# Kernel tuning notes

Hardware: AMD Instinct MI355X
Metric: run time of the kernel (lower is better)

The kernel has to match this reference:

```python
import jax, jax.numpy as jnp
import numpy as np

EMBED = 1024
DFF = 4096


def _layernorm(x, g, b, eps=1e-5):
    mu = jnp.mean(x, axis=-1, keepdims=True)
    var = jnp.var(x, axis=-1, keepdims=True)
    return (x - mu) * jax.lax.rsqrt(var + eps) * g + b


def setup_inputs() -> dict:
    key = jax.random.key(0)
    ks = jax.random.split(key, 14)
    s = 1.0 / np.sqrt(EMBED)
    sf = 1.0 / np.sqrt(DFF)
    d = {
        "src": jax.random.normal(ks[0], (4, 2048, EMBED), dtype=jnp.float32),
        "Wq": jax.random.uniform(ks[1], (EMBED, EMBED), jnp.float32, -s, s),
        "bq": jnp.zeros((EMBED,), jnp.float32),
        "Wk": jax.random.uniform(ks[2], (EMBED, EMBED), jnp.float32, -s, s),
        "bk": jnp.zeros((EMBED,), jnp.float32),
        "Wv": jax.random.uniform(ks[3], (EMBED, EMBED), jnp.float32, -s, s),
        "bv": jnp.zeros((EMBED,), jnp.float32),
        "Wo": jax.random.uniform(ks[4], (EMBED, EMBED), jnp.float32, -s, s),
        "bo": jnp.zeros((EMBED,), jnp.float32),
        "W1": jax.random.uniform(ks[5], (EMBED, DFF), jnp.float32, -s, s),
        "b1": jnp.zeros((DFF,), jnp.float32),
        "W2": jax.random.uniform(ks[6], (DFF, EMBED), jnp.float32, -sf, sf),
        "b2": jnp.zeros((EMBED,), jnp.float32),
        "g1": jnp.ones((EMBED,), jnp.float32),
        "be1": jnp.zeros((EMBED,), jnp.float32),
        "g2": jnp.ones((EMBED,), jnp.float32),
        "be2": jnp.zeros((EMBED,), jnp.float32),
    }
    return d


def reference(src, Wq, bq, Wk, bk, Wv, bv, Wo, bo, W1, b1, W2, b2, g1, be1, g2, be2):
    # Q/K/V projections: [b, s, d]
    Q = src @ Wq + bq
    K = src @ Wk + bk
    V = src @ Wv + bv
    # Single-head, UNSCALED attention (faithful to source: no 1/sqrt(d), num_heads unused)
    scores = jnp.einsum("bqd,bkd->bqk", Q, K)  # [b, s, s]
    weights = jax.nn.softmax(scores, axis=-1)
    attn = jnp.einsum("bqk,bkd->bqd", weights, V)
    attn = attn @ Wo + bo
    x = _layernorm(src + attn, g1, be1)
    ff = jax.nn.relu(x @ W1 + b1) @ W2 + b2
    return _layernorm(x + ff, g2, be2)
```

## Files before the change

kernel.cpp:

```cpp
#include <hip/hip_runtime.h>
#include <stdint.h>

typedef unsigned short u16;
typedef _Float16 v8h __attribute__((ext_vector_type(8)));
typedef float v4f __attribute__((ext_vector_type(4)));

static __device__ __forceinline__ float h2f(u16 u) {
    union { u16 s; _Float16 h; } v; v.s = u; return (float)v.h;
}
static __device__ __forceinline__ u16 f2h(float f) {
    union { u16 s; _Float16 h; } v; v.h = (_Float16)f; return v.s;
}

static __device__ __forceinline__ void gload_lds16(const u16* g, const u16* l) {
    __builtin_amdgcn_global_load_lds(
        (const __attribute__((address_space(1))) uint32_t*)(uintptr_t)g,
        (__attribute__((address_space(3))) uint32_t*)(uintptr_t)l,
        16, 0, 0);
}

__global__ __launch_bounds__(256) void cvt_f16(const float* __restrict__ in,
                                               u16* __restrict__ out, int n8) {
    const int i = blockIdx.x * 256 + threadIdx.x;
    if (i >= n8) return;
    const float4 a = ((const float4*)in)[2 * i];
    const float4 b = ((const float4*)in)[2 * i + 1];
    u16 o[8] = {f2h(a.x), f2h(a.y), f2h(a.z), f2h(a.w),
                f2h(b.x), f2h(b.y), f2h(b.z), f2h(b.w)};
    *(uint4*)(out + (size_t)i * 8) = *(const uint4*)o;
}

__global__ __launch_bounds__(256) void transpose_all(
    const float* __restrict__ Wq, const float* __restrict__ Wk,
    const float* __restrict__ Wv, const float* __restrict__ Wo,
    const float* __restrict__ W1, const float* __restrict__ W2,
    u16* __restrict__ WqkvT, u16* __restrict__ WoT,
    u16* __restrict__ W1T, u16* __restrict__ W2T)
{
    int t = blockIdx.x;
    const float* in; u16* out; long ldi, ldo; int xt;
    if (t < 1024)      {            in = Wq; out = WqkvT;               ldi = 1024; ldo = 1024; xt = 32; }
    else if (t < 2048) { t -= 1024; in = Wk; out = WqkvT + 1024*1024;   ldi = 1024; ldo = 1024; xt = 32; }
    else if (t < 3072) { t -= 2048; in = Wv; out = WqkvT + 2*1024*1024; ldi = 1024; ldo = 1024; xt = 32; }
    else if (t < 4096) { t -= 3072; in = Wo; out = WoT;                 ldi = 1024; ldo = 1024; xt = 32; }
    else if (t < 8192) { t -= 4096; in = W1; out = W1T;                 ldi = 4096; ldo = 1024; xt = 128; }
    else               { t -= 8192; in = W2; out = W2T;                 ldi = 1024; ldo = 4096; xt = 32; }
    const int c0 = (t % xt) * 32, r0 = (t / xt) * 32;
    __shared__ float tile[32][33];
    for (int i = threadIdx.y; i < 32; i += 8)
        tile[i][threadIdx.x] = in[(long)(r0 + i) * ldi + c0 + threadIdx.x];
    __syncthreads();
    for (int i = threadIdx.y; i < 32; i += 8)
        out[(long)(c0 + i) * ldo + r0 + threadIdx.x] = f2h(tile[threadIdx.x][i]);
}

template<int OMODE, int BIAS, bool RELU, int NX, int NY, int NZ>
__global__ __launch_bounds__(256, 2) void gemm256n(
    const u16* __restrict__ A, long lda, long Asb,
    const u16* __restrict__ B, long ldb, long Bsb,
    void* __restrict__ Cv, long ldc, long Csb, u16* __restrict__ C1,
    const float* __restrict__ bias, const float* __restrict__ bias2,
    const float* __restrict__ bias3, int K)
{
    constexpr int NWG = NX * NY * NZ;
    static_assert(NWG % 8 == 0, "XCD swizzle needs nwg % 8 == 0");
    alignas(16) __shared__ u16 As[4 * 8192];
    alignas(16) __shared__ u16 Bs[2 * 4096];

    const int tid = threadIdx.x;
    const int lane = tid & 63, wave = tid >> 6;
    const int l16 = lane & 15, quad = lane >> 4;
    const int wm = wave >> 1;
    const int wn = wave & 1;

    const int lin = blockIdx.x;
    const int tl = (lin & 7) * (NWG / 8) + (lin >> 3);
    const int xe = tl % NX;
    const int ye = (tl / NX) % NY;
    const int zb = tl / (NX * NY);
    const long m0 = (long)ye * 256;
    const long n0 = (long)xe * 128;

    const u16* Aop = A + (long)zb * Asb;
    const u16* Bop = B + (long)zb * Bsb;

    const int srow = tid >> 2;
    const int sq = (tid & 3) ^ ((tid >> 3) & 3);
    const long gaofs0 = (m0 + srow) * lda + sq * 8;
    const long gbofs0 = (n0 + srow) * ldb + sq * 8;
    const int wv512n = wave * 512;

    const int swzE = (quad ^ ((l16 >> 1) & 3)) * 8;
    const int aRow = (wm * 128 + l16) * 32 + swzE;
    const int bRow = (wn * 64 + l16) * 32 + swzE;

    v4f acc[8][4];
#pragma unroll
    for (int i = 0; i < 8; ++i)
#pragma unroll
        for (int j = 0; j < 4; ++j)
            acc[i][j] = (v4f){0.f, 0.f, 0.f, 0.f};
    v8h bf[4];

#define STAGE_A(RIDX, KP) do { \
        u16* lb_ = As + (RIDX) * 8192 + wv512n; \
        gload_lds16(Aop + gaofs0 + (KP), lb_); \
        gload_lds16(Aop + gaofs0 + 64 * lda + (KP), lb_ + 2048); \
        gload_lds16(Aop + gaofs0 + 128 * lda + (KP), lb_ + 4096); \
        gload_lds16(Aop + gaofs0 + 192 * lda + (KP), lb_ + 6144); } while (0)
#define STAGE_B(SLOT, KP) do { \
        u16* lb_ = Bs + (SLOT) * 4096 + wv512n; \
        gload_lds16(Bop + gbofs0 + (KP), lb_); \
        gload_lds16(Bop + gbofs0 + 64 * ldb + (KP), lb_ + 2048); } while (0)

#define PHASE(BUF, KH, CH, EVENW, STG) { \
        const u16* Ar_ = As + ((BUF) * 2 + (KH)) * 8192 + aRow + (CH) * 2048; \
        v8h af0 = *(const v8h*)(Ar_); \
        v8h af1 = *(const v8h*)(Ar_ + 512); \
        v8h af2 = *(const v8h*)(Ar_ + 1024); \
        v8h af3 = *(const v8h*)(Ar_ + 1536); \
        if ((CH) == 0) { \
            const u16* Br_ = Bs + (KH) * 4096 + bRow; \
            bf[0] = *(const v8h*)(Br_); \
            bf[1] = *(const v8h*)(Br_ + 512); \
            bf[2] = *(const v8h*)(Br_ + 1024); \
            bf[3] = *(const v8h*)(Br_ + 1536); \
        } \
        STG; \
        __builtin_amdgcn_s_barrier(); \
        asm volatile("s_waitcnt lgkmcnt(0)" ::: "memory"); \
        __builtin_amdgcn_s_setprio(1); \
        acc[(CH)*4+0][0] = __builtin_amdgcn_mfma_f32_16x16x32_f16(af0, bf[0], acc[(CH)*4+0][0], 0, 0, 0); \
        acc[(CH)*4+0][1] = __builtin_amdgcn_mfma_f32_16x16x32_f16(af0, bf[1], acc[(CH)*4+0][1], 0, 0, 0); \
        acc[(CH)*4+0][2] = __builtin_amdgcn_mfma_f32_16x16x32_f16(af0, bf[2], acc[(CH)*4+0][2], 0, 0, 0); \
        acc[(CH)*4+0][3] = __builtin_amdgcn_mfma_f32_16x16x32_f16(af0, bf[3], acc[(CH)*4+0][3], 0, 0, 0); \
        acc[(CH)*4+1][0] = __builtin_amdgcn_mfma_f32_16x16x32_f16(af1, bf[0], acc[(CH)*4+1][0], 0, 0, 0); \
        acc[(CH)*4+1][1] = __builtin_amdgcn_mfma_f32_16x16x32_f16(af1, bf[1], acc[(CH)*4+1][1], 0, 0, 0); \
        acc[(CH)*4+1][2] = __builtin_amdgcn_mfma_f32_16x16x32_f16(af1, bf[2], acc[(CH)*4+1][2], 0, 0, 0); \
        acc[(CH)*4+1][3] = __builtin_amdgcn_mfma_f32_16x16x32_f16(af1, bf[3], acc[(CH)*4+1][3], 0, 0, 0); \
        acc[(CH)*4+2][0] = __builtin_amdgcn_mfma_f32_16x16x32_f16(af2, bf[0], acc[(CH)*4+2][0], 0, 0, 0); \
        acc[(CH)*4+2][1] = __builtin_amdgcn_mfma_f32_16x16x32_f16(af2, bf[1], acc[(CH)*4+2][1], 0, 0, 0); \
        acc[(CH)*4+2][2] = __builtin_amdgcn_mfma_f32_16x16x32_f16(af2, bf[2], acc[(CH)*4+2][2], 0, 0, 0); \
        acc[(CH)*4+2][3] = __builtin_amdgcn_mfma_f32_16x16x32_f16(af2, bf[3], acc[(CH)*4+2][3], 0, 0, 0); \
        acc[(CH)*4+3][0] = __builtin_amdgcn_mfma_f32_16x16x32_f16(af3, bf[0], acc[(CH)*4+3][0], 0, 0, 0); \
        acc[(CH)*4+3][1] = __builtin_amdgcn_mfma_f32_16x16x32_f16(af3, bf[1], acc[(CH)*4+3][1], 0, 0, 0); \
        acc[(CH)*4+3][2] = __builtin_amdgcn_mfma_f32_16x16x32_f16(af3, bf[2], acc[(CH)*4+3][2], 0, 0, 0); \
        acc[(CH)*4+3][3] = __builtin_amdgcn_mfma_f32_16x16x32_f16(af3, bf[3], acc[(CH)*4+3][3], 0, 0, 0); \
        __builtin_amdgcn_s_setprio(0); \
        if (EVENW) asm volatile("s_waitcnt vmcnt(6)" ::: "memory"); \
        __builtin_amdgcn_s_barrier(); \
    }

    STAGE_A(0, 0);  STAGE_B(0, 0);
    STAGE_A(1, 32); STAGE_B(1, 32);
    STAGE_A(2, 64);
    asm volatile("s_waitcnt vmcnt(10)" ::: "memory");
    __builtin_amdgcn_s_barrier();

    const int NT = K >> 7;
#pragma unroll 1
    for (int t = 0; t < NT; ++t) {
        const long kb = (long)t * 128;
        long kp2  = kb + 128; if (kp2  >= K) kp2  = 0;
        long kp2b = kb + 160; if (kp2b >= K) kp2b = 0;
        long kp3  = kb + 192; if (kp3  >= K) kp3  = 0;

        PHASE(0, 0, 0, false, STAGE_A(3, kb + 96))
        PHASE(0, 0, 1, true,  STAGE_B(0, kb + 64))
        PHASE(0, 1, 0, false, STAGE_A(0, kp2))
        PHASE(0, 1, 1, true,  STAGE_B(1, kb + 96))
        PHASE(1, 0, 0, false, STAGE_A(1, kp2b))
        PHASE(1, 0, 1, true,  STAGE_B(0, kp2))
        PHASE(1, 1, 0, false, STAGE_A(2, kp3))
        PHASE(1, 1, 1, true,  STAGE_B(1, kp2b))
    }

    asm volatile("s_waitcnt vmcnt(0) lgkmcnt(0)" ::: "memory");
    __builtin_amdgcn_s_barrier();

#undef PHASE
#undef STAGE_A
#undef STAGE_B

    float bv[4];
#pragma unroll
    for (int j = 0; j < 4; ++j) {
        const long col = n0 + wn * 64 + j * 16 + l16;
        if (BIAS == 0) bv[j] = 0.f;
        else if (BIAS == 1) bv[j] = bias[col];
        else {
            const int sel = (int)(col >> 10);
            const float* bp = sel == 0 ? bias : (sel == 1 ? bias2 : bias3);
            bv[j] = bp[col & 1023];
        }
    }

    if (OMODE == 3 && n0 >= 2048) {
        const long bb = m0 >> 11, mb = m0 & 2047;
        u16* C = C1 + bb * Csb;
#pragma unroll
        for (int j = 0; j < 4; ++j) {
            const long col = n0 - 2048 + wn * 64 + j * 16 + l16;
            u16* pc = C + col * 2048 + mb + wm * 128 + quad * 4;
#pragma unroll
            for (int i = 0; i < 8; ++i) {
                u16 o[4];
#pragma unroll
                for (int r = 0; r < 4; ++r) {
                    float val = acc[i][j][r] + bv[j];
                    if (RELU) val = fmaxf(val, 0.f);
                    o[r] = f2h(val);
                }
                *(uint2*)(pc + i * 16) = *(const uint2*)o;
            }
        }
    } else {
        const long cb = (OMODE == 3 ? 0 : (long)zb * Csb)
                      + (m0 + wm * 128 + quad * 4) * ldc + (n0 + wn * 64 + l16);
        u16* p0 = (u16*)Cv + cb;
#pragma unroll
        for (int i = 0; i < 8; ++i)
#pragma unroll
            for (int r = 0; r < 4; ++r) {
                u16* prow = p0 + (long)(i * 16 + r) * ldc;
#pragma unroll
                for (int j = 0; j < 4; ++j) {
                    float val = acc[i][j][r] + bv[j];
                    if (RELU) val = fmaxf(val, 0.f);
                    prow[j * 16] = f2h(val);
                }
            }
    }
}

__global__ __launch_bounds__(256) void softmax_rows(u16* __restrict__ S) {
    const long row = blockIdx.x;
    u16* p = S + row * 2048;
    const int t = threadIdx.x;
    const int lane = t & 63, wv = t >> 6;

    union { uint4 u; u16 h[8]; } ld;
    ld.u = *(const uint4*)(p + t * 8);
    float v[8];
    float mx = -1e30f;
#pragma unroll
    for (int i = 0; i < 8; ++i) { v[i] = h2f(ld.h[i]); mx = fmaxf(mx, v[i]); }
#pragma unroll
    for (int o = 1; o < 64; o <<= 1) mx = fmaxf(mx, __shfl_xor(mx, o, 64));
    __shared__ float cw[4], cs[4];
    if (lane == 0) cw[wv] = mx;
    __syncthreads();
    mx = fmaxf(fmaxf(cw[0], cw[1]), fmaxf(cw[2], cw[3]));

    float sum = 0.f;
#pragma unroll
    for (int i = 0; i < 8; ++i) { v[i] = __expf(v[i] - mx); sum += v[i]; }
#pragma unroll
    for (int o = 1; o < 64; o <<= 1) sum += __shfl_xor(sum, o, 64);
    if (lane == 0) cs[wv] = sum;
    __syncthreads();
    sum = (cs[0] + cs[1]) + (cs[2] + cs[3]);

    const float inv = 1.f / sum;
#pragma unroll
    for (int i = 0; i < 8; ++i) ld.h[i] = f2h(v[i] * inv);
    *(uint4*)(p + t * 8) = ld.u;
}

__global__ __launch_bounds__(256) void ln_one(
    const float* __restrict__ a, const u16* __restrict__ bb,
    const float* __restrict__ g, const float* __restrict__ be,
    u16* __restrict__ out16)
{
    const long base = (long)blockIdx.x * 1024;
    const int t = threadIdx.x;
    const int lane = t & 63, wv = t >> 6;
    const int c0 = t * 4;

    const float4 av = *(const float4*)(a + base + c0);
    union { uint2 u; u16 h[4]; } bv;
    bv.u = *(const uint2*)(bb + base + c0);
    float v[4] = {av.x + h2f(bv.h[0]), av.y + h2f(bv.h[1]),
                  av.z + h2f(bv.h[2]), av.w + h2f(bv.h[3])};
    float s = 0.f, ss = 0.f;
#pragma unroll
    for (int i = 0; i < 4; ++i) { s += v[i]; ss += v[i] * v[i]; }
#pragma unroll
    for (int o = 1; o < 64; o <<= 1) { s += __shfl_xor(s, o, 64); ss += __shfl_xor(ss, o, 64); }
    __shared__ float cs[4], css[4];
    if (lane == 0) { cs[wv] = s; css[wv] = ss; }
    __syncthreads();
    s  = (cs[0] + cs[1]) + (cs[2] + cs[3]);
    ss = (css[0] + css[1]) + (css[2] + css[3]);

    const float mean = s * (1.f / 1024.f);
    const float var = ss * (1.f / 1024.f) - mean * mean;
    const float rstd = rsqrtf(var + 1e-5f);
    const float4 gv = *(const float4*)(g + c0);
    const float4 bev = *(const float4*)(be + c0);
    u16 o[4] = {f2h((v[0] - mean) * rstd * gv.x + bev.x),
                f2h((v[1] - mean) * rstd * gv.y + bev.y),
                f2h((v[2] - mean) * rstd * gv.z + bev.z),
                f2h((v[3] - mean) * rstd * gv.w + bev.w)};
    *(uint2*)(out16 + base + c0) = *(const uint2*)o;
}

__global__ __launch_bounds__(256) void ln_two(
    const u16* __restrict__ a, const u16* __restrict__ bb,
    const float* __restrict__ g, const float* __restrict__ be,
    float* __restrict__ out)
{
    const long base = (long)blockIdx.x * 1024;
    const int t = threadIdx.x;
    const int lane = t & 63, wv = t >> 6;
    const int c0 = t * 4;

    union { uint2 u; u16 h[4]; } avu, bvu;
    avu.u = *(const uint2*)(a + base + c0);
    bvu.u = *(const uint2*)(bb + base + c0);
    float v[4];
    float s = 0.f, ss = 0.f;
#pragma unroll
    for (int i = 0; i < 4; ++i) {
        v[i] = h2f(avu.h[i]) + h2f(bvu.h[i]);
        s += v[i]; ss += v[i] * v[i];
    }
#pragma unroll
    for (int o = 1; o < 64; o <<= 1) { s += __shfl_xor(s, o, 64); ss += __shfl_xor(ss, o, 64); }
    __shared__ float cs[4], css[4];
    if (lane == 0) { cs[wv] = s; css[wv] = ss; }
    __syncthreads();
    s  = (cs[0] + cs[1]) + (cs[2] + cs[3]);
    ss = (css[0] + css[1]) + (css[2] + css[3]);

    const float mean = s * (1.f / 1024.f);
    const float var = ss * (1.f / 1024.f) - mean * mean;
    const float rstd = rsqrtf(var + 1e-5f);
    const float4 gv = *(const float4*)(g + c0);
    const float4 bev = *(const float4*)(be + c0);
    float4 o;
    o.x = (v[0] - mean) * rstd * gv.x + bev.x;
    o.y = (v[1] - mean) * rstd * gv.y + bev.y;
    o.z = (v[2] - mean) * rstd * gv.z + bev.z;
    o.w = (v[3] - mean) * rstd * gv.w + bev.w;
    *(float4*)(out + base + c0) = o;
}

extern "C" void kernel_launch(void* const* d_in, const int* in_sizes, int n_in,
                              void* d_out, int out_size, void* d_ws, size_t ws_size,
                              hipStream_t stream) {
    (void)in_sizes; (void)n_in; (void)out_size; (void)ws_size;
    constexpr long S = 2048, E = 1024, F = 4096, M = 8192;

    const float* src = (const float*)d_in[0];
    const float* Wq  = (const float*)d_in[1];
    const float* bq  = (const float*)d_in[2];
    const float* Wk  = (const float*)d_in[3];
    const float* bk  = (const float*)d_in[4];
    const float* Wv  = (const float*)d_in[5];
    const float* bv  = (const float*)d_in[6];
    const float* Wo  = (const float*)d_in[7];
    const float* bo  = (const float*)d_in[8];
    const float* W1  = (const float*)d_in[9];
    const float* b1  = (const float*)d_in[10];
    const float* W2  = (const float*)d_in[11];
    const float* b2  = (const float*)d_in[12];
    const float* g1  = (const float*)d_in[13];
    const float* be1 = (const float*)d_in[14];
    const float* g2  = (const float*)d_in[15];
    const float* be2 = (const float*)d_in[16];

    char* ws = (char*)d_ws;
    size_t off = 0;
    auto take = [&](size_t bytes) {
        char* p = ws + off;
        off += (bytes + 255) & ~(size_t)255;
        return p;
    };
    const size_t MB16 = 16777216;
    u16*   srcH  = (u16*)take(MB16);
    u16*   WqkvT = (u16*)take(3 * E * E * 2);
    u16*   WoT   = (u16*)take(E * E * 2);
    u16*   W1T   = (u16*)take(F * E * 2);
    u16*   W2T   = (u16*)take(E * F * 2);
    char*  B0    = take(2 * MB16);
    char*  B1    = take(MB16);
    char*  B2    = take(4ull * S * S * 4);
    char*  B3    = take(MB16);
    char*  B4    = take(MB16);

    u16*   QK    = (u16*)B0;
    u16*   VT    = (u16*)B1;
    u16*   Sh    = (u16*)B2;
    u16*   hf    = (u16*)B2;
    u16*   attn  = (u16*)B3;
    u16*   xh    = (u16*)B3;
    u16*   attnO = (u16*)B4;
    u16*   ffO   = (u16*)B4;

    dim3 blk(256), tb(32, 8);

    cvt_f16<<<dim3(M * E / 8 / 256), blk, 0, stream>>>(src, srcH, M * E / 8);

    transpose_all<<<dim3(12288), tb, 0, stream>>>(Wq, Wk, Wv, Wo, W1, W2,
                                                  WqkvT, WoT, W1T, W2T);

    gemm256n<3, 3, false, 24, 32, 1><<<dim3(24 * 32), blk, 0, stream>>>(
        srcH, E, 0, WqkvT, E, 0, QK, 2 * E, E * S, VT, bq, bk, bv, E);

    gemm256n<0, 0, false, 16, 8, 4><<<dim3(16 * 8 * 4), blk, 0, stream>>>(
        QK, 2 * E, S * 2 * E, QK + E, 2 * E, S * 2 * E,
        Sh, S, S * S, nullptr, nullptr, nullptr, nullptr, E);

    softmax_rows<<<dim3(M), blk, 0, stream>>>(Sh);

    gemm256n<0, 0, false, 8, 8, 4><<<dim3(8 * 8 * 4), blk, 0, stream>>>(
        Sh, S, S * S, VT, S, E * S,
        attn, E, S * E, nullptr, nullptr, nullptr, nullptr, S);

    gemm256n<0, 1, false, 8, 32, 1><<<dim3(8 * 32), blk, 0, stream>>>(
        attn, E, 0, WoT, E, 0, attnO, E, 0, nullptr, bo, nullptr, nullptr, E);

    ln_one<<<dim3(M), blk, 0, stream>>>(src, attnO, g1, be1, xh);

    gemm256n<0, 1, true, 32, 32, 1><<<dim3(32 * 32), blk, 0, stream>>>(
        xh, E, 0, W1T, E, 0, hf, F, 0, nullptr, b1, nullptr, nullptr, E);

    gemm256n<0, 1, false, 8, 32, 1><<<dim3(8 * 32), blk, 0, stream>>>(
        hf, F, 0, W2T, F, 0, ffO, E, 0, nullptr, b2, nullptr, nullptr, F);

    ln_two<<<dim3(M), blk, 0, stream>>>(xh, ffO, g2, be2, (float*)d_out);
}
```

Baseline: 478.7 us.

## Add 256x256-tile 512-thread pipelined GEMM for the FFN up-projection

Introduces gemmQ, a new 8-wave kernel with 256x256 output tiles, four-slot LDS ring buffers for A and B, and eight phases per K-step that interleave direct-to-LDS global loads with MFMA work and raise wave priority around the MFMAs. It replaces the previous 256-thread kernel for the W1 GEMM with bias and ReLU, cutting the grid from 1024 to 512 workgroups. The aim is more operand reuse per tile and better overlap of memory loads with matrix math. In exchange it uses 128 KB of LDS, carries a larger accumulator set per thread, and relies on hand-tuned waitcnt and barrier ordering that could be fragile.

After: 488.0 us. About the same (+1.9%).

```diff
diff --git a/kernel.cpp b/kernel.cpp
--- a/kernel.cpp
+++ b/kernel.cpp
@@ -52,6 +52,144 @@
     __syncthreads();
     for (int i = threadIdx.y; i < 32; i += 8)
         out[(long)(c0 + i) * ldo + r0 + threadIdx.x] = f2h(tile[threadIdx.x][i]);
+}
+
+template<int BIAS, bool RELU, int NX, int NY>
+__global__ __launch_bounds__(512, 2) void gemmQ(
+    const u16* __restrict__ A, long lda,
+    const u16* __restrict__ B, long ldb,
+    u16* __restrict__ C, long ldc,
+    const float* __restrict__ bias, int K)
+{
+    constexpr int NWG = NX * NY;
+    static_assert(NWG % 8 == 0, "XCD swizzle needs nwg % 8 == 0");
+    alignas(16) __shared__ u16 As[4 * 8192];
+    alignas(16) __shared__ u16 Bs[4 * 8192];
+
+    const int tid = threadIdx.x;
+    const int lane = tid & 63, wave = tid >> 6;
+    const int l16 = lane & 15, quad = lane >> 4;
+    const int wr = wave >> 2;
+    const int wc = wave & 3;
+
+    const int lin = blockIdx.x;
+    const int tl = (lin & 7) * (NWG / 8) + (lin >> 3);
+    const int xe = tl % NX, ye = tl / NX;
+    const long m0 = (long)ye * 256, n0 = (long)xe * 256;
+
+    const int srow = tid >> 3;
+    const int sg = (tid & 7) ^ ((tid >> 3) & 7);
+    const long gA = (m0 + srow) * lda + sg * 8;
+    const long gB = (n0 + srow) * ldb + sg * 8;
+
+    const int sl0 = (quad ^ (l16 & 7)) * 8;
+    const int aoff = (wr * 64 + l16) * 64 + sl0;
+    const int boff = (wc * 32 + l16) * 64 + sl0;
+
+    v4f acc[8][4];
+#pragma unroll
+    for (int i = 0; i < 8; ++i)
+#pragma unroll
+        for (int j = 0; j < 4; ++j)
+            acc[i][j] = (v4f){0.f, 0.f, 0.f, 0.f};
+
+#define STAGE_A(RIDX, HALF, KP) do { \
+        u16* d_ = As + (RIDX) * 8192 + wave * 512; \
+        gload_lds16(A + gA + (long)((HALF) * 128) * lda + (KP), d_); \
+        gload_lds16(A + gA + (long)((HALF) * 128 + 64) * lda + (KP), d_ + 4096); } while (0)
+#define STAGE_B(RIDX, HALF, KP) do { \
+        u16* d_ = Bs + (RIDX) * 8192 + wave * 512; \
+        gload_lds16(B + gB + (long)((HALF) * 128) * ldb + (KP), d_); \
+        gload_lds16(B + gB + (long)((HALF) * 128 + 64) * ldb + (KP), d_ + 4096); } while (0)
+
+#define MF8(KC, MH, NH) \
+    acc[(MH)*4+0][(NH)*2+0] = __builtin_amdgcn_mfma_f32_16x16x32_f16(a##KC##0, b##KC##0, acc[(MH)*4+0][(NH)*2+0], 0, 0, 0); \
+    acc[(MH)*4+0][(NH)*2+1] = __builtin_amdgcn_mfma_f32_16x16x32_f16(a##KC##0, b##KC##1, acc[(MH)*4+0][(NH)*2+1], 0, 0, 0); \
+    acc[(MH)*4+1][(NH)*2+0] = __builtin_amdgcn_mfma_f32_16x16x32_f16(a##KC##1, b##KC##0, acc[(MH)*4+1][(NH)*2+0], 0, 0, 0); \
+    acc[(MH)*4+1][(NH)*2+1] = __builtin_amdgcn_mfma_f32_16x16x32_f16(a##KC##1, b##KC##1, acc[(MH)*4+1][(NH)*2+1], 0, 0, 0); \
+    acc[(MH)*4+2][(NH)*2+0] = __builtin_amdgcn_mfma_f32_16x16x32_f16(a##KC##2, b##KC##0, acc[(MH)*4+2][(NH)*2+0], 0, 0, 0); \
+    acc[(MH)*4+2][(NH)*2+1] = __builtin_amdgcn_mfma_f32_16x16x32_f16(a##KC##2, b##KC##1, acc[(MH)*4+2][(NH)*2+1], 0, 0, 0); \
+    acc[(MH)*4+3][(NH)*2+0] = __builtin_amdgcn_mfma_f32_16x16x32_f16(a##KC##3, b##KC##0, acc[(MH)*4+3][(NH)*2+0], 0, 0, 0); \
+    acc[(MH)*4+3][(NH)*2+1] = __builtin_amdgcn_mfma_f32_16x16x32_f16(a##KC##3, b##KC##1, acc[(MH)*4+3][(NH)*2+1], 0, 0, 0);
+
+#define PHASE(BUF, MH, NH, WV, STG) { \
+        const u16* Ar_ = As + ((BUF) * 2 + (MH)) * 8192; \
+        const u16* Br_ = Bs + ((BUF) * 2 + (NH)) * 8192; \
+        v8h a00 = *(const v8h*)(Ar_ + aoff); \
+        v8h a01 = *(const v8h*)(Ar_ + aoff + 1024); \
+        v8h a02 = *(const v8h*)(Ar_ + aoff + 2048); \
+        v8h a03 = *(const v8h*)(Ar_ + aoff + 3072); \
+        v8h b00 = *(const v8h*)(Br_ + boff); \
+        v8h b01 = *(const v8h*)(Br_ + boff + 1024); \
+        v8h a10 = *(const v8h*)(Ar_ + (aoff ^ 32)); \
+        v8h a11 = *(const v8h*)(Ar_ + ((aoff + 1024) ^ 32)); \
+        v8h a12 = *(const v8h*)(Ar_ + ((aoff + 2048) ^ 32)); \
+        v8h a13 = *(const v8h*)(Ar_ + ((aoff + 3072) ^ 32)); \
+        v8h b10 = *(const v8h*)(Br_ + (boff ^ 32)); \
+        v8h b11 = *(const v8h*)(Br_ + ((boff + 1024) ^ 32)); \
+        STG; \
+        __builtin_amdgcn_s_barrier(); \
+        asm volatile("s_waitcnt lgkmcnt(0)" ::: "memory"); \
+        __builtin_amdgcn_s_setprio(1); \
+        MF8(0, MH, NH) \
+        MF8(1, MH, NH) \
+        __builtin_amdgcn_s_setprio(0); \
+        if (WV) asm volatile("s_waitcnt vmcnt(6)" ::: "memory"); \
+        __builtin_amdgcn_s_barrier(); \
+    }
+
+    STAGE_A(0, 0, 0); STAGE_B(0, 0, 0);
+    STAGE_A(1, 1, 0); STAGE_B(1, 1, 0);
+    STAGE_A(2, 0, 64); STAGE_B(2, 0, 64);
+    asm volatile("s_waitcnt vmcnt(4)" ::: "memory");
+    __builtin_amdgcn_s_barrier();
+
+    const int NT = K >> 7;
+#pragma unroll 1
+    for (int t = 0; t < NT; ++t) {
+        const long kb = (long)t * 128;
+        const long kp1 = kb + 64;
+        long kp2 = kb + 128; if (kp2 >= K) kp2 = 0;
+        long kp3 = kb + 192; if (kp3 >= K) kp3 = 0;
+
+        PHASE(0, 0, 0, false, STAGE_A(3, 1, kp1))
+        PHASE(0, 0, 1, false, STAGE_B(3, 1, kp1))
+        PHASE(0, 1, 0, false, STAGE_A(0, 0, kp2))
+        PHASE(0, 1, 1, true,  STAGE_B(0, 0, kp2))
+        PHASE(1, 0, 0, false, STAGE_A(1, 1, kp2))
+        PHASE(1, 0, 1, false, STAGE_B(1, 1, kp2))
+        PHASE(1, 1, 0, false, STAGE_A(2, 0, kp3))
+        PHASE(1, 1, 1, true,  STAGE_B(2, 0, kp3))
+    }
+
+    asm volatile("s_waitcnt vmcnt(0) lgkmcnt(0)" ::: "memory");
+    __builtin_amdgcn_s_barrier();
+
+#undef PHASE
+#undef MF8
+#undef STAGE_A
+#undef STAGE_B
+
+    float bv[4];
+#pragma unroll
+    for (int jj = 0; jj < 4; ++jj) {
+        const long col = n0 + (jj >> 1) * 128 + wc * 32 + (jj & 1) * 16 + l16;
+        bv[jj] = (BIAS == 1) ? bias[col] : 0.f;
+    }
+
+#pragma unroll
+    for (int ii = 0; ii < 8; ++ii)
+#pragma unroll
+        for (int r = 0; r < 4; ++r) {
+            const long row = m0 + (ii >> 2) * 128 + wr * 64 + (ii & 3) * 16 + quad * 4 + r;
+            u16* prow = C + row * ldc + n0 + l16;
+#pragma unroll
+            for (int jj = 0; jj < 4; ++jj) {
+                float val = acc[ii][jj][r] + bv[jj];
+                if (RELU) val = fmaxf(val, 0.f);
+                prow[(jj >> 1) * 128 + wc * 32 + (jj & 1) * 16] = f2h(val);
+            }
+        }
 }
 
 template<int OMODE, int BIAS, bool RELU, int NX, int NY, int NZ>
@@ -398,7 +536,7 @@
     u16*   attnO = (u16*)B4;
     u16*   ffO   = (u16*)B4;
 
-    dim3 blk(256), tb(32, 8);
+    dim3 blk(256), blk5(512), tb(32, 8);
 
     cvt_f16<<<dim3(M * E / 8 / 256), blk, 0, stream>>>(src, srcH, M * E / 8);
 
@@ -423,8 +561,8 @@
 
     ln_one<<<dim3(M), blk, 0, stream>>>(src, attnO, g1, be1, xh);
 
-    gemm256n<0, 1, true, 32, 32, 1><<<dim3(32 * 32), blk, 0, stream>>>(
-        xh, E, 0, W1T, E, 0, hf, F, 0, nullptr, b1, nullptr, nullptr, E);
+    gemmQ<1, true, 16, 32><<<dim3(16 * 32), blk5, 0, stream>>>(
+        xh, E, W1T, E, hf, F, b1, E);
 
     gemm256n<0, 1, false, 8, 32, 1><<<dim3(8 * 32), blk, 0, stream>>>(
         hf, F, 0, W2T, F, 0, ffO, E, 0, nullptr, b2, nullptr, nullptr, F);
```
